# Kernel tuning notes

Hardware: AMD Instinct MI355X
Metric: run time of the kernel (lower is better)

The kernel has to match this reference:

```python
import jax, jax.numpy as jnp
import numpy as np

# Hierarchy: 3 levels with 50 / 500 / 5000 classes, branching factor 10.
PIQUETS = (0, 50, 550, 5550)  # cumulative offsets per level
NB_LEVELS = 3
BATCH = 4096


def _make_parent():
    """parent[j] = global index of the parent of global node j (0 for roots).
    Encodes the same structure as the dense H matrix (H[p, j] = 1 iff parent[j] == p)."""
    parent = np.zeros(PIQUETS[-1], dtype=np.int32)
    parent[PIQUETS[1]:PIQUETS[2]] = np.arange(500) // 10            # level-1 -> level-0
    parent[PIQUETS[2]:PIQUETS[3]] = PIQUETS[1] + np.arange(5000) // 10  # level-2 -> level-1
    return jnp.asarray(parent)


def setup_inputs() -> dict:
    key = jax.random.key(0)
    k1, k2 = jax.random.split(key)
    y_pred = jax.random.normal(k1, (BATCH, PIQUETS[-1]), dtype=jnp.float32)
    target = jax.random.randint(k2, (BATCH,), 0, 5000)  # local leaf-level indices
    return {"y_pred": y_pred, "target": target, "parent": _make_parent()}


def reference(y_pred, target, parent):
    # children_preds[b, p] = sum of child logits of node p
    # == (H[:piquets[-2], :] @ y_pred.T).T, exploiting H's one-parent sparsity.
    children = jax.ops.segment_sum(
        y_pred.T[PIQUETS[1]:], parent[PIQUETS[1]:], num_segments=PIQUETS[-2]
    ).T  # (B, piquets[-2])

    levels_pred = [y_pred[:, PIQUETS[k]:PIQUETS[k + 1]] for k in range(NB_LEVELS)]
    levels_children = [children[:, PIQUETS[k]:PIQUETS[k + 1]] for k in range(NB_LEVELS - 1)]
    log_p = [jax.nn.log_softmax(l, axis=1) for l in levels_pred]
    log_c = [jax.nn.log_softmax(l, axis=1) for l in levels_children]

    # Ancestor targets per level (vectorized replacement for get_grandparents loops)
    g = target.astype(jnp.int32) + PIQUETS[-2]  # global leaf index
    globs = [g]
    for _ in range(NB_LEVELS - 1):
        globs.append(parent[globs[-1]])
    globs = globs[::-1]  # level 0 .. level L-1, global indices
    loc = [globs[k] - PIQUETS[k] for k in range(NB_LEVELS)]  # local per-level targets

    def ce(logp, tgt):
        return -jnp.take_along_axis(logp, tgt[:, None], axis=1).mean()

    def kl_mean(logp, logq):
        # torch KLDivLoss(reduction='mean'): mean over ALL elements of q*(log q - log p)
        return jnp.mean(jnp.exp(logq) * (logq - logp))

    loss = jnp.float32(0.0)
    kl_penalty = jnp.float32(0.0)
    for k in range(NB_LEVELS - 1):
        kl_penalty += 0.5 * (kl_mean(log_p[k], log_c[k]) + kl_mean(log_c[k], log_p[k]))
        loss += 0.5 * ce(log_p[k], loc[k])
    loss += 0.5 * ce(log_p[-1], loc[-1])
    loss += 0.5 * kl_penalty
    return loss
```

## Files before the change

kernel.cpp:

```cpp
#include <hip/hip_runtime.h>

#define BATCH 4096
#define ROW   5550

__device__ __forceinline__ void lse_combine(float& m, float& s, float m2, float s2) {
    float mn = fmaxf(m, m2);
    s = s * __expf(m - mn) + s2 * __expf(m2 - mn);
    m = mn;
}

__device__ __forceinline__ void wave_lse(float& m, float& s) {
    #pragma unroll
    for (int off = 32; off; off >>= 1) {
        float m2 = __shfl_xor(m, off, 64);
        float s2 = __shfl_xor(s, off, 64);
        lse_combine(m, s, m2, s2);
    }
}

__device__ __forceinline__ float wave_sum(float v) {
    #pragma unroll
    for (int off = 32; off; off >>= 1) v += __shfl_xor(v, off, 64);
    return v;
}

__device__ __forceinline__ void block_lse(float& m, float& s, float* scr, int tid) {
    wave_lse(m, s);
    int wid = tid >> 6;
    if ((tid & 63) == 0) { scr[wid * 2] = m; scr[wid * 2 + 1] = s; }
    __syncthreads();
    float M = scr[0], S = scr[1];
    lse_combine(M, S, scr[2], scr[3]);
    lse_combine(M, S, scr[4], scr[5]);
    lse_combine(M, S, scr[6], scr[7]);
    __syncthreads();
    m = M; s = S;
}

__device__ __forceinline__ float block_sum(float v, float* scr, int tid) {
    v = wave_sum(v);
    if ((tid & 63) == 0) scr[tid >> 6] = v;
    __syncthreads();
    float r = scr[0] + scr[1] + scr[2] + scr[3];
    __syncthreads();
    return r;
}

__global__ void zero_kernel(float* out) { out[0] = 0.0f; }

__global__ __launch_bounds__(256)
void hjsd_kernel(const float* __restrict__ y, const int* __restrict__ tgt,
                 float* __restrict__ out) {
    __shared__ float s_c1[500];
    __shared__ float s_scr[8];

    const int b   = blockIdx.x;
    const int tid = threadIdx.x;
    const float* yrow = y + (size_t)b * ROW;

    float m2 = -1e30f, s2 = 0.0f;
    float mc1 = -1e30f, sc1 = 0.0f;
    if (tid < 250) {
        const float2* p = reinterpret_cast<const float2*>(yrow + 550 + 20 * tid);
        float v[20];
        #pragma unroll
        for (int j = 0; j < 10; ++j) {
            float2 t2 = p[j];
            v[2 * j] = t2.x; v[2 * j + 1] = t2.y;
        }
        float c[2];
        #pragma unroll
        for (int g = 0; g < 2; ++g) {
            float sum = 0.0f, mx = -1e30f;
            #pragma unroll
            for (int j = 0; j < 10; ++j) { float x = v[10 * g + j]; sum += x; mx = fmaxf(mx, x); }
            float se = 0.0f;
            #pragma unroll
            for (int j = 0; j < 10; ++j) se += __expf(v[10 * g + j] - mx);
            lse_combine(m2, s2, mx, se);
            c[g] = sum;
            s_c1[2 * tid + g] = sum;
        }
        mc1 = fmaxf(c[0], c[1]);
        sc1 = __expf(c[0] - mc1) + __expf(c[1] - mc1);
    }
    block_lse(m2, s2, s_scr, tid);
    block_lse(mc1, sc1, s_scr, tid);

    float x1[10];
    float m1 = -1e30f, s1 = 0.0f, mc0 = -1e30f, sc0 = 0.0f;
    float c0v = 0.0f, x0 = 0.0f;
    if (tid < 50) {
        const float2* p = reinterpret_cast<const float2*>(yrow + 50 + 10 * tid);
        #pragma unroll
        for (int j = 0; j < 5; ++j) {
            float2 t2 = p[j];
            x1[2 * j] = t2.x; x1[2 * j + 1] = t2.y;
        }
        float sum = 0.0f, mx = -1e30f;
        #pragma unroll
        for (int j = 0; j < 10; ++j) { sum += x1[j]; mx = fmaxf(mx, x1[j]); }
        float se = 0.0f;
        #pragma unroll
        for (int j = 0; j < 10; ++j) se += __expf(x1[j] - mx);
        m1 = mx; s1 = se;
        c0v = sum;
        mc0 = sum; sc0 = 1.0f;
        x0 = yrow[tid];
    }
    block_lse(m1, s1, s_scr, tid);
    block_lse(mc0, sc0, s_scr, tid);

    float m0 = (tid < 50) ? x0 : -1e30f;
    float s0 = (tid < 50) ? 1.0f : 0.0f;
    block_lse(m0, s0, s_scr, tid);

    float L2  = m2  + __logf(s2);
    float LC1 = mc1 + __logf(sc1);
    float L1  = m1  + __logf(s1);
    float LC0 = mc0 + __logf(sc0);
    float L0  = m0  + __logf(s0);

    float part = 0.0f;
    if (tid < 50) {
        float S11 = 0.0f, S21 = 0.0f;
        #pragma unroll
        for (int j = 0; j < 10; ++j) {
            float x = x1[j];
            float c = s_c1[10 * tid + j];
            S11 += __expf(c - LC1) * (c - x);
            S21 += __expf(x - L1)  * (x - c);
        }
        float c = c0v;
        float x = x0;
        float S10 = __expf(c - LC0) * (c - x);
        float S20 = __expf(x - L0)  * (x - c);
        part = (0.25f / 500.0f) * (S11 + S21) + (0.25f / 50.0f) * (S10 + S20);
    }
    float Ssum = block_sum(part, s_scr, tid);

    if (tid == 0) {
        int t = tgt[b];
        float ce0 = L0 - yrow[t / 100];
        float ce1 = L1 - yrow[50 + t / 10];
        float ce2 = L2 - yrow[550 + t];
        float row = 0.5f * (ce0 + ce1 + ce2) + Ssum;
        atomicAdd(out, row * (1.0f / BATCH));
    }
}

extern "C" void kernel_launch(void* const* d_in, const int* in_sizes, int n_in,
                              void* d_out, int out_size, void* d_ws, size_t ws_size,
                              hipStream_t stream) {
    const float* y   = (const float*)d_in[0];
    const int*   tgt = (const int*)d_in[1];
    float* out = (float*)d_out;

    zero_kernel<<<1, 1, 0, stream>>>(out);
    hjsd_kernel<<<BATCH, 256, 0, stream>>>(y, tgt, out);
}
```

Before: 169.5 us.

## Stage rows in LDS, batch block reductions, replace atomics with two-pass reduce

Each block now copies its whole 5550-float row into shared memory with coalesced float2 loads before computing, instead of strided per-thread global loads. The five separate block-level log-sum-exp reductions, each with two barriers, are merged into one shared-memory exchange. The per-row global atomicAdd and the zero kernel are replaced by writing per-row results to workspace, followed by a single-block reduce kernel. This costs about 22 KB of LDS per block, which limits occupancy, and adds a second dependent launch.

```diff
diff --git a/kernel.cpp b/kernel.cpp
--- a/kernel.cpp
+++ b/kernel.cpp
@@ -24,129 +24,134 @@
     return v;
 }
 
-__device__ __forceinline__ void block_lse(float& m, float& s, float* scr, int tid) {
-    wave_lse(m, s);
-    int wid = tid >> 6;
-    if ((tid & 63) == 0) { scr[wid * 2] = m; scr[wid * 2 + 1] = s; }
-    __syncthreads();
-    float M = scr[0], S = scr[1];
-    lse_combine(M, S, scr[2], scr[3]);
-    lse_combine(M, S, scr[4], scr[5]);
-    lse_combine(M, S, scr[6], scr[7]);
-    __syncthreads();
-    m = M; s = S;
-}
-
-__device__ __forceinline__ float block_sum(float v, float* scr, int tid) {
-    v = wave_sum(v);
-    if ((tid & 63) == 0) scr[tid >> 6] = v;
-    __syncthreads();
-    float r = scr[0] + scr[1] + scr[2] + scr[3];
-    __syncthreads();
-    return r;
-}
-
-__global__ void zero_kernel(float* out) { out[0] = 0.0f; }
-
 __global__ __launch_bounds__(256)
 void hjsd_kernel(const float* __restrict__ y, const int* __restrict__ tgt,
-                 float* __restrict__ out) {
+                 float* __restrict__ rowout) {
+    __shared__ float s_row[ROW];
     __shared__ float s_c1[500];
-    __shared__ float s_scr[8];
+    __shared__ float s_scr[48];
 
     const int b   = blockIdx.x;
     const int tid = threadIdx.x;
-    const float* yrow = y + (size_t)b * ROW;
+
+    const float2* prow  = reinterpret_cast<const float2*>(y + (size_t)b * ROW);
+    float2*       srow2 = reinterpret_cast<float2*>(s_row);
+    for (int i = tid; i < ROW / 2; i += 256) srow2[i] = prow[i];
+    __syncthreads();
 
     float m2 = -1e30f, s2 = 0.0f;
     float mc1 = -1e30f, sc1 = 0.0f;
     if (tid < 250) {
-        const float2* p = reinterpret_cast<const float2*>(yrow + 550 + 20 * tid);
+        const float2* p = reinterpret_cast<const float2*>(s_row + 550 + 20 * tid);
         float v[20];
         #pragma unroll
-        for (int j = 0; j < 10; ++j) {
-            float2 t2 = p[j];
-            v[2 * j] = t2.x; v[2 * j + 1] = t2.y;
-        }
-        float c[2];
+        for (int j = 0; j < 10; ++j) { float2 t2 = p[j]; v[2*j] = t2.x; v[2*j+1] = t2.y; }
+        float c0 = 0.f, c1 = 0.f, mx0 = -1e30f, mx1 = -1e30f;
         #pragma unroll
-        for (int g = 0; g < 2; ++g) {
-            float sum = 0.0f, mx = -1e30f;
-            #pragma unroll
-            for (int j = 0; j < 10; ++j) { float x = v[10 * g + j]; sum += x; mx = fmaxf(mx, x); }
-            float se = 0.0f;
-            #pragma unroll
-            for (int j = 0; j < 10; ++j) se += __expf(v[10 * g + j] - mx);
-            lse_combine(m2, s2, mx, se);
-            c[g] = sum;
-            s_c1[2 * tid + g] = sum;
-        }
-        mc1 = fmaxf(c[0], c[1]);
-        sc1 = __expf(c[0] - mc1) + __expf(c[1] - mc1);
+        for (int j = 0; j < 10; ++j) { c0 += v[j];      mx0 = fmaxf(mx0, v[j]); }
+        #pragma unroll
+        for (int j = 0; j < 10; ++j) { c1 += v[10 + j]; mx1 = fmaxf(mx1, v[10 + j]); }
+        float se0 = 0.f, se1 = 0.f;
+        #pragma unroll
+        for (int j = 0; j < 10; ++j) se0 += __expf(v[j]      - mx0);
+        #pragma unroll
+        for (int j = 0; j < 10; ++j) se1 += __expf(v[10 + j] - mx1);
+        lse_combine(m2, s2, mx0, se0);
+        lse_combine(m2, s2, mx1, se1);
+        s_c1[2 * tid]     = c0;
+        s_c1[2 * tid + 1] = c1;
+        mc1 = fmaxf(c0, c1);
+        sc1 = __expf(c0 - mc1) + __expf(c1 - mc1);
     }
-    block_lse(m2, s2, s_scr, tid);
-    block_lse(mc1, sc1, s_scr, tid);
 
     float x1[10];
     float m1 = -1e30f, s1 = 0.0f, mc0 = -1e30f, sc0 = 0.0f;
     float c0v = 0.0f, x0 = 0.0f;
     if (tid < 50) {
-        const float2* p = reinterpret_cast<const float2*>(yrow + 50 + 10 * tid);
+        const float2* p = reinterpret_cast<const float2*>(s_row + 50 + 10 * tid);
         #pragma unroll
-        for (int j = 0; j < 5; ++j) {
-            float2 t2 = p[j];
-            x1[2 * j] = t2.x; x1[2 * j + 1] = t2.y;
-        }
-        float sum = 0.0f, mx = -1e30f;
+        for (int j = 0; j < 5; ++j) { float2 t2 = p[j]; x1[2*j] = t2.x; x1[2*j+1] = t2.y; }
+        float sum = 0.f, mx = -1e30f;
         #pragma unroll
         for (int j = 0; j < 10; ++j) { sum += x1[j]; mx = fmaxf(mx, x1[j]); }
-        float se = 0.0f;
+        float se = 0.f;
         #pragma unroll
         for (int j = 0; j < 10; ++j) se += __expf(x1[j] - mx);
         m1 = mx; s1 = se;
         c0v = sum;
         mc0 = sum; sc0 = 1.0f;
-        x0 = yrow[tid];
+        x0 = s_row[tid];
     }
-    block_lse(m1, s1, s_scr, tid);
-    block_lse(mc0, sc0, s_scr, tid);
-
     float m0 = (tid < 50) ? x0 : -1e30f;
     float s0 = (tid < 50) ? 1.0f : 0.0f;
-    block_lse(m0, s0, s_scr, tid);
 
-    float L2  = m2  + __logf(s2);
-    float LC1 = mc1 + __logf(sc1);
-    float L1  = m1  + __logf(s1);
-    float LC0 = mc0 + __logf(sc0);
-    float L0  = m0  + __logf(s0);
+    wave_lse(m2, s2); wave_lse(mc1, sc1); wave_lse(m1, s1);
+    wave_lse(mc0, sc0); wave_lse(m0, s0);
+    const int wid = tid >> 6;
+    if ((tid & 63) == 0) {
+        float* w = s_scr + wid * 10;
+        w[0] = m2;  w[1] = s2;
+        w[2] = mc1; w[3] = sc1;
+        w[4] = m1;  w[5] = s1;
+        w[6] = mc0; w[7] = sc0;
+        w[8] = m0;  w[9] = s0;
+    }
+    __syncthreads();
+    float L[5];
+    #pragma unroll
+    for (int k = 0; k < 5; ++k) {
+        float M = s_scr[2 * k], S = s_scr[2 * k + 1];
+        lse_combine(M, S, s_scr[10 + 2 * k], s_scr[11 + 2 * k]);
+        lse_combine(M, S, s_scr[20 + 2 * k], s_scr[21 + 2 * k]);
+        lse_combine(M, S, s_scr[30 + 2 * k], s_scr[31 + 2 * k]);
+        L[k] = M + __logf(S);
+    }
 
     float part = 0.0f;
     if (tid < 50) {
-        float S11 = 0.0f, S21 = 0.0f;
+        const float L2v = L[0], LC1 = L[1], L1v = L[2], LC0 = L[3], L0v = L[4];
+        (void)L2v;
+        float S11 = 0.f, S21 = 0.f;
         #pragma unroll
         for (int j = 0; j < 10; ++j) {
             float x = x1[j];
             float c = s_c1[10 * tid + j];
             S11 += __expf(c - LC1) * (c - x);
-            S21 += __expf(x - L1)  * (x - c);
+            S21 += __expf(x - L1v) * (x - c);
         }
-        float c = c0v;
-        float x = x0;
-        float S10 = __expf(c - LC0) * (c - x);
-        float S20 = __expf(x - L0)  * (x - c);
+        float S10 = __expf(c0v - LC0) * (c0v - x0);
+        float S20 = __expf(x0  - L0v) * (x0 - c0v);
         part = (0.25f / 500.0f) * (S11 + S21) + (0.25f / 50.0f) * (S10 + S20);
     }
-    float Ssum = block_sum(part, s_scr, tid);
+    __syncthreads();
+    part = wave_sum(part);
+    if ((tid & 63) == 0) s_scr[tid >> 6] = part;
+    __syncthreads();
 
     if (tid == 0) {
+        float Ssum = s_scr[0] + s_scr[1] + s_scr[2] + s_scr[3];
         int t = tgt[b];
-        float ce0 = L0 - yrow[t / 100];
-        float ce1 = L1 - yrow[50 + t / 10];
-        float ce2 = L2 - yrow[550 + t];
-        float row = 0.5f * (ce0 + ce1 + ce2) + Ssum;
-        atomicAdd(out, row * (1.0f / BATCH));
+        float ce0 = L[4] - s_row[t / 100];
+        float ce1 = L[2] - s_row[50 + t / 10];
+        float ce2 = L[0] - s_row[550 + t];
+        rowout[b] = 0.5f * (ce0 + ce1 + ce2) + Ssum;
     }
+}
+
+__global__ __launch_bounds__(256)
+void reduce_kernel(const float* __restrict__ rows, float* __restrict__ out) {
+    __shared__ float scr[4];
+    const int tid = threadIdx.x;
+    const float4* p = reinterpret_cast<const float4*>(rows);
+    float s = 0.0f;
+    for (int i = tid; i < BATCH / 4; i += 256) {
+        float4 v = p[i];
+        s += v.x + v.y + v.z + v.w;
+    }
+    s = wave_sum(s);
+    if ((tid & 63) == 0) scr[tid >> 6] = s;
+    __syncthreads();
+    if (tid == 0) out[0] = (scr[0] + scr[1] + scr[2] + scr[3]) * (1.0f / BATCH);
 }
 
 extern "C" void kernel_launch(void* const* d_in, const int* in_sizes, int n_in,
@@ -154,8 +159,9 @@
                               hipStream_t stream) {
     const float* y   = (const float*)d_in[0];
     const int*   tgt = (const int*)d_in[1];
-    float* out = (float*)d_out;
+    float* out    = (float*)d_out;
+    float* rowbuf = (float*)d_ws;
 
-    zero_kernel<<<1, 1, 0, stream>>>(out);
-    hjsd_kernel<<<BATCH, 256, 0, stream>>>(y, tgt, out);
+    hjsd_kernel<<<BATCH, 256, 0, stream>>>(y, tgt, rowbuf);
+    reduce_kernel<<<1, 256, 0, stream>>>(rowbuf, out);
 }
```

Result: faster. 150.3 us (-11.4%).
